# Kernel tuning notes

Measured on AMD Instinct MI355X. Metric: run time of the kernel, lower is better.

Reference implementation:

```python
import jax, jax.numpy as jnp
import numpy as np

N_NODES = 50000
N_EDGES = 800000
D_IN = 128
D_OUT = 128

def setup_inputs() -> dict:
    key = jax.random.key(0)
    k1, k2, k3, k4, k5, k6 = jax.random.split(key, 6)
    adj_row = jax.random.randint(k1, (N_EDGES,), 0, N_NODES, dtype=jnp.int32)
    adj_col = jax.random.randint(k2, (N_EDGES,), 0, N_NODES, dtype=jnp.int32)
    adj_vals = jax.random.uniform(k3, (N_EDGES,), dtype=jnp.float32)
    features = jax.random.normal(k4, (N_NODES, D_IN), dtype=jnp.float32)
    W = jax.random.normal(k5, (D_OUT, D_IN), dtype=jnp.float32) * (1.0 / np.sqrt(D_IN))
    b = jax.random.normal(k6, (D_OUT,), dtype=jnp.float32) * 0.01
    return {"adj_row": adj_row, "adj_col": adj_col, "adj_vals": adj_vals,
            "features": features, "W": W, "b": b}

def reference(adj_row, adj_col, adj_vals, features, W, b):
    # SpMM: f[i] = sum_{e: row[e]=i} vals[e] * features[col[e]]
    msgs = adj_vals[:, None] * features[adj_col]          # [E, D_IN]
    f = jax.ops.segment_sum(msgs, adj_row, num_segments=N_NODES)  # [N, D_IN]
    # dense linear: f @ W.T + b  (nn.Linear convention)
    out = jnp.einsum('nd,od->no', f, W) + b               # [N, D_OUT]
    return out
```

## Files before the change

### kernel.cpp

```cpp
#include <hip/hip_runtime.h>
#include <hip/hip_fp16.h>

#define N_NODES 50000
#define N_EDGES 800000
#define D 128
#define PAD 56
#define NPART 8
#define NCHUNK 391

typedef __attribute__((ext_vector_type(8))) short bf16x8;
typedef __attribute__((ext_vector_type(4))) float f32x4;

#define WS_H_OFF      0
#define WS_ECSR_OFF   12800000
#define WS_COUNTS_OFF 24000000
#define WS_REC_OFF    24200000

__device__ __forceinline__ unsigned int f2bf(float f) {
    unsigned int u = __float_as_uint(f);
    unsigned int r = u + 0x7FFFu + ((u >> 16) & 1u);
    return r >> 16;
}
__device__ __forceinline__ float bf_lo(unsigned int u) {
    return __uint_as_float(u << 16);
}
__device__ __forceinline__ float bf_hi(unsigned int u) {
    return __uint_as_float(u & 0xFFFF0000u);
}
__device__ __forceinline__ int part_of(unsigned int row) {
    return (int)((row * 687195ull) >> 32);
}

__global__ void pack_rec_kernel(const int* __restrict__ row,
                                const int* __restrict__ col,
                                const float* __restrict__ vals,
                                int2* __restrict__ rec,
                                int* __restrict__ counts) {
    int i = blockIdx.x * blockDim.x + threadIdx.x;
    if (i < N_NODES) counts[i] = 0;
    int e = i * 4;
    if (e >= N_EDGES) return;
    int4   rr = *reinterpret_cast<const int4*>(row + e);
    int4   cc = *reinterpret_cast<const int4*>(col + e);
    float4 vv = *reinterpret_cast<const float4*>(vals + e);
    rec[e + 0] = make_int2((rr.x << 16) | cc.x, __float_as_int(vv.x));
    rec[e + 1] = make_int2((rr.y << 16) | cc.y, __float_as_int(vv.y));
    rec[e + 2] = make_int2((rr.z << 16) | cc.z, __float_as_int(vv.z));
    rec[e + 3] = make_int2((rr.w << 16) | cc.w, __float_as_int(vv.w));
}

__global__ __launch_bounds__(256) void csr_build_kernel(
        const int2* __restrict__ rec, int* __restrict__ counts,
        unsigned int* __restrict__ ecsr) {
    const int p     = blockIdx.x & 7;
    const int chunk = blockIdx.x >> 3;
    const int t     = threadIdx.x;

    #pragma unroll
    for (int i = 0; i < 8; ++i) {
        int e = chunk * 2048 + i * 256 + t;
        if (e < N_EDGES) {
            int2 r = rec[e];
            unsigned int row = ((unsigned int)r.x) >> 16;
            if (part_of(row) == p) {
                int k = atomicAdd(&counts[row], 1);
                unsigned int c16 = (unsigned int)r.x & 0xFFFFu;
                unsigned int h = __half_as_ushort(__float2half_rn(__int_as_float(r.y)));
                if (k < PAD) ecsr[row * PAD + k] = c16 | (h << 16);
            }
        }
    }
}

__global__ __launch_bounds__(256) void gemm_mfma_kernel(
        const float* __restrict__ X, const float* __restrict__ W,
        unsigned int* __restrict__ H16) {
    __shared__ unsigned int Wlds[128 * 64];
    const int t = threadIdx.x;

    char* lw = (char*)Wlds;
    #pragma unroll
    for (int i = 0; i < 16; ++i) {
        int idx4 = t + i * 256;
        float4 w4 = reinterpret_cast<const float4*>(W)[idx4];
        int row = idx4 >> 5;
        int kq  = idx4 & 31;
        int byte = (row * 256 + kq * 8) ^ ((row & 7) << 4);
        uint2 p;
        p.x = f2bf(w4.x) | (f2bf(w4.y) << 16);
        p.y = f2bf(w4.z) | (f2bf(w4.w) << 16);
        *reinterpret_cast<uint2*>(lw + byte) = p;
    }
    __syncthreads();

    const int w    = t >> 6;
    const int lane = t & 63;
    const int lrow = lane & 15;
    const int lk   = lane >> 4;
    const int base = blockIdx.x * 128;

    const int xr0 = base + w * 16 + lrow;
    const int xr1 = base + 64 + w * 16 + lrow;
    const int xr0c = (xr0 < N_NODES) ? xr0 : (N_NODES - 1);
    const int xr1c = (xr1 < N_NODES) ? xr1 : (N_NODES - 1);

    const float4* Xr0 = reinterpret_cast<const float4*>(X + (size_t)xr0c * D);
    const float4* Xr1 = reinterpret_cast<const float4*>(X + (size_t)xr1c * D);
    bf16x8 xb0[4], xb1[4];
    #pragma unroll
    for (int ks = 0; ks < 4; ++ks) {
        float4 a0 = Xr0[ks * 8 + lk * 2];
        float4 b0 = Xr0[ks * 8 + lk * 2 + 1];
        float4 a1 = Xr1[ks * 8 + lk * 2];
        float4 b1 = Xr1[ks * 8 + lk * 2 + 1];
        bf16x8 v0, v1;
        v0[0] = (short)f2bf(a0.x); v0[1] = (short)f2bf(a0.y);
        v0[2] = (short)f2bf(a0.z); v0[3] = (short)f2bf(a0.w);
        v0[4] = (short)f2bf(b0.x); v0[5] = (short)f2bf(b0.y);
        v0[6] = (short)f2bf(b0.z); v0[7] = (short)f2bf(b0.w);
        v1[0] = (short)f2bf(a1.x); v1[1] = (short)f2bf(a1.y);
        v1[2] = (short)f2bf(a1.z); v1[3] = (short)f2bf(a1.w);
        v1[4] = (short)f2bf(b1.x); v1[5] = (short)f2bf(b1.y);
        v1[6] = (short)f2bf(b1.z); v1[7] = (short)f2bf(b1.w);
        xb0[ks] = v0;
        xb1[ks] = v1;
    }

    const char* lr = (const char*)Wlds;
    #pragma unroll
    for (int n0 = 0; n0 < 8; ++n0) {
        f32x4 acc0 = {0.f, 0.f, 0.f, 0.f};
        f32x4 acc1 = {0.f, 0.f, 0.f, 0.f};
        #pragma unroll
        for (int ks = 0; ks < 4; ++ks) {
            int wrow = n0 * 16 + lrow;
            int byte = (wrow * 256 + ks * 64 + lk * 16) ^ ((wrow & 7) << 4);
            bf16x8 af = *reinterpret_cast<const bf16x8*>(lr + byte);
            acc0 = __builtin_amdgcn_mfma_f32_16x16x32_bf16(af, xb0[ks], acc0, 0, 0, 0);
            acc1 = __builtin_amdgcn_mfma_f32_16x16x32_bf16(af, xb1[ks], acc1, 0, 0, 0);
        }
        if (xr0 < N_NODES) {
            uint2 p;
            p.x = f2bf(acc0[0]) | (f2bf(acc0[1]) << 16);
            p.y = f2bf(acc0[2]) | (f2bf(acc0[3]) << 16);
            *reinterpret_cast<uint2*>(H16 + (size_t)xr0 * 64 + n0 * 8 + (lk << 1)) = p;
        }
        if (xr1 < N_NODES) {
            uint2 p;
            p.x = f2bf(acc1[0]) | (f2bf(acc1[1]) << 16);
            p.y = f2bf(acc1[2]) | (f2bf(acc1[3]) << 16);
            *reinterpret_cast<uint2*>(H16 + (size_t)xr1 * 64 + n0 * 8 + (lk << 1)) = p;
        }
    }
}

__global__ __launch_bounds__(256) void aggregate_kernel(
        const int* __restrict__ counts, const unsigned int* __restrict__ ecsr,
        const unsigned int* __restrict__ H16,
        const float* __restrict__ b, float* __restrict__ out) {
    int gtid = blockIdx.x * blockDim.x + threadIdx.x;
    int row  = gtid >> 6;
    int lane = threadIdx.x & 63;
    if (row >= N_NODES) return;

    const int eg = lane >> 4;
    const int c  = lane & 15;

    int deg = counts[row];
    if (deg > PAD) deg = PAD;
    const unsigned int* seg = ecsr + row * PAD;

    float a[8];
    #pragma unroll
    for (int k = 0; k < 8; ++k) a[k] = 0.f;

    #define EDGE_BODY(IDX)                                                        \
        {                                                                         \
            unsigned int rc = seg[(IDX)];                                         \
            int   cx = rc & 0xFFFFu;                                              \
            float v  = __half2float(__ushort_as_half((unsigned short)(rc >> 16)));\
            uint4 h = *reinterpret_cast<const uint4*>(H16 + (size_t)cx * 64 + c * 4);\
            a[0] += v * bf_lo(h.x); a[1] += v * bf_hi(h.x);                       \
            a[2] += v * bf_lo(h.y); a[3] += v * bf_hi(h.y);                       \
            a[4] += v * bf_lo(h.z); a[5] += v * bf_hi(h.z);                       \
            a[6] += v * bf_lo(h.w); a[7] += v * bf_hi(h.w);                       \
        }

    int i = eg;
    for (; i + 4 < deg; i += 8) {
        EDGE_BODY(i);
        EDGE_BODY(i + 4);
    }
    if (i < deg) EDGE_BODY(i);
    #undef EDGE_BODY

    #pragma unroll
    for (int k = 0; k < 8; ++k) {
        a[k] += __shfl_xor(a[k], 16, 64);
        a[k] += __shfl_xor(a[k], 32, 64);
    }

    if (eg == 0) {
        float4 b0 = *reinterpret_cast<const float4*>(b + c * 8);
        float4 b1 = *reinterpret_cast<const float4*>(b + c * 8 + 4);
        float4 o0 = {a[0] + b0.x, a[1] + b0.y, a[2] + b0.z, a[3] + b0.w};
        float4 o1 = {a[4] + b1.x, a[5] + b1.y, a[6] + b1.z, a[7] + b1.w};
        float* dst = out + (size_t)row * D + c * 8;
        *reinterpret_cast<float4*>(dst)     = o0;
        *reinterpret_cast<float4*>(dst + 4) = o1;
    }
}

extern "C" void kernel_launch(void* const* d_in, const int* in_sizes, int n_in,
                              void* d_out, int out_size, void* d_ws, size_t ws_size,
                              hipStream_t stream) {
    const int*   adj_row  = (const int*)d_in[0];
    const int*   adj_col  = (const int*)d_in[1];
    const float* adj_vals = (const float*)d_in[2];
    const float* features = (const float*)d_in[3];
    const float* W        = (const float*)d_in[4];
    const float* b        = (const float*)d_in[5];
    float*       out      = (float*)d_out;

    char* ws = (char*)d_ws;
    unsigned int* H16    = (unsigned int*)(ws + WS_H_OFF);
    unsigned int* ecsr   = (unsigned int*)(ws + WS_ECSR_OFF);
    int*          counts = (int*)(ws + WS_COUNTS_OFF);
    int2*         rec    = (int2*)(ws + WS_REC_OFF);

    pack_rec_kernel<<<(N_EDGES / 4 + 255) / 256, 256, 0, stream>>>(
        adj_row, adj_col, adj_vals, rec, counts);
    csr_build_kernel<<<NCHUNK * NPART, 256, 0, stream>>>(rec, counts, ecsr);
    gemm_mfma_kernel<<<(N_NODES + 127) / 128, 256, 0, stream>>>(features, W, H16);
    {
        int blocks = (N_NODES * 64 + 255) / 256;
        aggregate_kernel<<<blocks, 256, 0, stream>>>(counts, ecsr, H16, b, out);
    }
}
```

Baseline: 93.10 us.

## Merge edge packing into GEMM launch and vectorize CSR build record loads

Folds the edge record packing and count zeroing into the GEMM kernel as extra blocks, so both independent stages run in one launch and overlap on the device. This removes a kernel launch and the gap between the two stages. The CSR build kernel now loads two records per thread with 16-byte loads instead of one 8-byte load. The cost is that GEMM blocks reserve LDS even when they only do packing, and the mixed grid may schedule unevenly.

```diff
diff --git a/kernel.cpp b/kernel.cpp
--- a/kernel.cpp
+++ b/kernel.cpp
@@ -7,6 +7,8 @@
 #define PAD 56
 #define NPART 8
 #define NCHUNK 391
+#define GEMM_BLOCKS 391
+#define PACK_BLOCKS 782
 
 typedef __attribute__((ext_vector_type(8))) short bf16x8;
 typedef __attribute__((ext_vector_type(4))) float f32x4;
@@ -31,61 +33,39 @@
     return (int)((row * 687195ull) >> 32);
 }
 
-__global__ void pack_rec_kernel(const int* __restrict__ row,
-                                const int* __restrict__ col,
-                                const float* __restrict__ vals,
-                                int2* __restrict__ rec,
-                                int* __restrict__ counts) {
-    int i = blockIdx.x * blockDim.x + threadIdx.x;
-    if (i < N_NODES) counts[i] = 0;
-    int e = i * 4;
-    if (e >= N_EDGES) return;
-    int4   rr = *reinterpret_cast<const int4*>(row + e);
-    int4   cc = *reinterpret_cast<const int4*>(col + e);
-    float4 vv = *reinterpret_cast<const float4*>(vals + e);
-    rec[e + 0] = make_int2((rr.x << 16) | cc.x, __float_as_int(vv.x));
-    rec[e + 1] = make_int2((rr.y << 16) | cc.y, __float_as_int(vv.y));
-    rec[e + 2] = make_int2((rr.z << 16) | cc.z, __float_as_int(vv.z));
-    rec[e + 3] = make_int2((rr.w << 16) | cc.w, __float_as_int(vv.w));
-}
-
-__global__ __launch_bounds__(256) void csr_build_kernel(
-        const int2* __restrict__ rec, int* __restrict__ counts,
-        unsigned int* __restrict__ ecsr) {
-    const int p     = blockIdx.x & 7;
-    const int chunk = blockIdx.x >> 3;
-    const int t     = threadIdx.x;
-
-    #pragma unroll
-    for (int i = 0; i < 8; ++i) {
-        int e = chunk * 2048 + i * 256 + t;
-        if (e < N_EDGES) {
-            int2 r = rec[e];
-            unsigned int row = ((unsigned int)r.x) >> 16;
-            if (part_of(row) == p) {
-                int k = atomicAdd(&counts[row], 1);
-                unsigned int c16 = (unsigned int)r.x & 0xFFFFu;
-                unsigned int h = __half_as_ushort(__float2half_rn(__int_as_float(r.y)));
-                if (k < PAD) ecsr[row * PAD + k] = c16 | (h << 16);
-            }
-        }
-    }
-}
-
-__global__ __launch_bounds__(256) void gemm_mfma_kernel(
+__global__ __launch_bounds__(256) void gemm_pack_kernel(
         const float* __restrict__ X, const float* __restrict__ W,
-        unsigned int* __restrict__ H16) {
+        unsigned int* __restrict__ H16,
+        const int* __restrict__ row, const int* __restrict__ col,
+        const float* __restrict__ vals,
+        int2* __restrict__ rec, int* __restrict__ counts) {
     __shared__ unsigned int Wlds[128 * 64];
     const int t = threadIdx.x;
+
+    if (blockIdx.x >= GEMM_BLOCKS) {
+        const int pb  = blockIdx.x - GEMM_BLOCKS;
+        const int gid = pb * 256 + t;
+        if (gid < N_NODES) counts[gid] = 0;
+        const int e = gid * 4;
+        if (e >= N_EDGES) return;
+        int4   rr = *reinterpret_cast<const int4*>(row + e);
+        int4   cc = *reinterpret_cast<const int4*>(col + e);
+        float4 vv = *reinterpret_cast<const float4*>(vals + e);
+        rec[e + 0] = make_int2((rr.x << 16) | cc.x, __float_as_int(vv.x));
+        rec[e + 1] = make_int2((rr.y << 16) | cc.y, __float_as_int(vv.y));
+        rec[e + 2] = make_int2((rr.z << 16) | cc.z, __float_as_int(vv.z));
+        rec[e + 3] = make_int2((rr.w << 16) | cc.w, __float_as_int(vv.w));
+        return;
+    }
 
     char* lw = (char*)Wlds;
     #pragma unroll
     for (int i = 0; i < 16; ++i) {
         int idx4 = t + i * 256;
         float4 w4 = reinterpret_cast<const float4*>(W)[idx4];
-        int row = idx4 >> 5;
-        int kq  = idx4 & 31;
-        int byte = (row * 256 + kq * 8) ^ ((row & 7) << 4);
+        int wr = idx4 >> 5;
+        int kq = idx4 & 31;
+        int byte = (wr * 256 + kq * 8) ^ ((wr & 7) << 4);
         uint2 p;
         p.x = f2bf(w4.x) | (f2bf(w4.y) << 16);
         p.y = f2bf(w4.z) | (f2bf(w4.w) << 16);
@@ -133,8 +113,8 @@
         f32x4 acc1 = {0.f, 0.f, 0.f, 0.f};
         #pragma unroll
         for (int ks = 0; ks < 4; ++ks) {
-            int wrow = n0 * 16 + lrow;
-            int byte = (wrow * 256 + ks * 64 + lk * 16) ^ ((wrow & 7) << 4);
+            int wr = n0 * 16 + lrow;
+            int byte = (wr * 256 + ks * 64 + lk * 16) ^ ((wr & 7) << 4);
             bf16x8 af = *reinterpret_cast<const bf16x8*>(lr + byte);
             acc0 = __builtin_amdgcn_mfma_f32_16x16x32_bf16(af, xb0[ks], acc0, 0, 0, 0);
             acc1 = __builtin_amdgcn_mfma_f32_16x16x32_bf16(af, xb1[ks], acc1, 0, 0, 0);
@@ -150,6 +130,36 @@
             p.x = f2bf(acc1[0]) | (f2bf(acc1[1]) << 16);
             p.y = f2bf(acc1[2]) | (f2bf(acc1[3]) << 16);
             *reinterpret_cast<uint2*>(H16 + (size_t)xr1 * 64 + n0 * 8 + (lk << 1)) = p;
+        }
+    }
+}
+
+__global__ __launch_bounds__(256) void csr_build_kernel(
+        const int2* __restrict__ rec, int* __restrict__ counts,
+        unsigned int* __restrict__ ecsr) {
+    const int p     = blockIdx.x & 7;
+    const int chunk = blockIdx.x >> 3;
+    const int t     = threadIdx.x;
+
+    #pragma unroll
+    for (int i = 0; i < 4; ++i) {
+        int e0 = chunk * 2048 + i * 512 + t * 2;
+        if (e0 < N_EDGES) {
+            int4 r2 = *reinterpret_cast<const int4*>(rec + e0);
+            unsigned int row0 = ((unsigned int)r2.x) >> 16;
+            unsigned int row1 = ((unsigned int)r2.z) >> 16;
+            if (part_of(row0) == p) {
+                int k = atomicAdd(&counts[row0], 1);
+                unsigned int c16 = (unsigned int)r2.x & 0xFFFFu;
+                unsigned int h = __half_as_ushort(__float2half_rn(__int_as_float(r2.y)));
+                if (k < PAD) ecsr[row0 * PAD + k] = c16 | (h << 16);
+            }
+            if (part_of(row1) == p) {
+                int k = atomicAdd(&counts[row1], 1);
+                unsigned int c16 = (unsigned int)r2.z & 0xFFFFu;
+                unsigned int h = __half_as_ushort(__float2half_rn(__int_as_float(r2.w)));
+                if (k < PAD) ecsr[row1 * PAD + k] = c16 | (h << 16);
+            }
         }
     }
 }
@@ -228,10 +238,9 @@
     int*          counts = (int*)(ws + WS_COUNTS_OFF);
     int2*         rec    = (int2*)(ws + WS_REC_OFF);
 
-    pack_rec_kernel<<<(N_EDGES / 4 + 255) / 256, 256, 0, stream>>>(
-        adj_row, adj_col, adj_vals, rec, counts);
+    gemm_pack_kernel<<<GEMM_BLOCKS + PACK_BLOCKS, 256, 0, stream>>>(
+        features, W, H16, adj_row, adj_col, adj_vals, rec, counts);
     csr_build_kernel<<<NCHUNK * NPART, 256, 0, stream>>>(rec, counts, ecsr);
-    gemm_mfma_kernel<<<(N_NODES + 127) / 128, 256, 0, stream>>>(features, W, H16);
     {
         int blocks = (N_NODES * 64 + 255) / 256;
         aggregate_kernel<<<blocks, 256, 0, stream>>>(counts, ecsr, H16, b, out);
```

Result: faster. 89.85 us (-3.5%).
